# Kernel optimization log

Measured on AMD Instinct MI355X. Metric: run time of the kernel, lower is better.

The kernel has to match this reference:

```python
import jax, jax.numpy as jnp
import numpy as np

B, S, DIM, H = 1, 4096, 1024, 16
HEAD_DIM = DIM // H
ROPE_THETA = 10000.0
LN_EPS = 1e-5


def _rope_cos_sin(seq_len, dim, theta):
    # frequencies over the FULL model dim (rope applied before head split, as in source)
    inv_freq = 1.0 / (theta ** (jnp.arange(0, dim, 2, dtype=jnp.float32) / dim))  # (dim/2,)
    ang = jnp.arange(seq_len, dtype=jnp.float32)[:, None] * inv_freq[None, :]     # (S, dim/2)
    cos = jnp.concatenate([jnp.cos(ang), jnp.cos(ang)], axis=-1)                  # (S, dim)
    sin = jnp.concatenate([jnp.sin(ang), jnp.sin(ang)], axis=-1)
    return cos, sin


def _rotate_half(x):
    d = x.shape[-1] // 2
    return jnp.concatenate([-x[..., d:], x[..., :d]], axis=-1)


def _apply_rope(x, cos, sin):
    # x: (B, S, dim); cos/sin: (S, dim)
    return x * cos[None] + _rotate_half(x) * sin[None]


def setup_inputs() -> dict:
    key = jax.random.key(0)
    ks = jax.random.split(key, 5)
    sc = 1.0 / np.sqrt(DIM)
    return {
        "x": jax.random.normal(ks[0], (B, S, DIM), dtype=jnp.float32),
        "Wqkv": jax.random.normal(ks[1], (DIM, 3 * DIM), dtype=jnp.float32) * sc,
        "bqkv": jax.random.normal(ks[2], (3 * DIM,), dtype=jnp.float32) * 0.01,
        "Wo": jax.random.normal(ks[3], (DIM, DIM), dtype=jnp.float32) * sc,
        "bo": jax.random.normal(ks[4], (DIM,), dtype=jnp.float32) * 0.01,
        "gamma": jnp.ones((DIM,), dtype=jnp.float32),
        "beta": jnp.zeros((DIM,), dtype=jnp.float32),
    }


def reference(x, Wqkv, bqkv, Wo, bo, gamma, beta):
    b, s, d = x.shape
    qkv = x @ Wqkv + bqkv                      # (B, S, 3*dim)
    q, k, v = jnp.split(qkv, 3, axis=-1)       # each (B, S, dim)
    cos, sin = _rope_cos_sin(s, d, ROPE_THETA)
    q = _apply_rope(q, cos, sin)
    k = _apply_rope(k, cos, sin)
    # split heads
    q = q.reshape(b, s, H, HEAD_DIM)
    k = k.reshape(b, s, H, HEAD_DIM)
    v = v.reshape(b, s, H, HEAD_DIM)
    scale = 1.0 / np.sqrt(HEAD_DIM)
    scores = jnp.einsum('bqhd,bkhd->bhqk', q, k) * scale  # (B, H, S, S)
    causal = jnp.triu(jnp.ones((s, s), dtype=bool), k=1)
    scores = jnp.where(causal[None, None], -jnp.inf, scores)
    attn = jax.nn.softmax(scores, axis=-1)
    out = jnp.einsum('bhqk,bkhd->bqhd', attn, v).reshape(b, s, d)
    out = out @ Wo + bo
    # LayerNorm (dropout is identity in eval mode)
    mu = jnp.mean(out, axis=-1, keepdims=True)
    var = jnp.mean(jnp.square(out - mu), axis=-1, keepdims=True)
    return (out - mu) * jax.lax.rsqrt(var + LN_EPS) * gamma + beta
```

## Files before the change

### kernel.cpp

```cpp
#include <hip/hip_runtime.h>
#include <cstdint>
#include <cstddef>

#define S_LEN 4096
#define DIM   1024
#define NH    16
#define HD    64
#define QKV_N 3072

typedef __attribute__((ext_vector_type(8))) short short8;
typedef __attribute__((ext_vector_type(4))) float f32x4;
typedef __attribute__((ext_vector_type(4))) unsigned short ushort4v;

__device__ inline unsigned short f2bf(float x) {
    unsigned int u = __builtin_bit_cast(unsigned int, x);
    u += 0x7fffu + ((u >> 16) & 1u);
    return (unsigned short)(u >> 16);
}

__device__ inline void gl_lds16(const void* g, void* l) {
    __builtin_amdgcn_global_load_lds(
        (const __attribute__((address_space(1))) void*)g,
        (__attribute__((address_space(3))) void*)l, 16, 0, 0);
}

__global__ __launch_bounds__(256) void gemm_mfma_kernel(
    const unsigned short* __restrict__ A,
    const unsigned short* __restrict__ Bt,
    const float* __restrict__ bias,
    float* __restrict__ C,
    int M, int N, int K)
{
    __shared__ unsigned short As[128 * 32];
    __shared__ unsigned short Bs[128 * 32];

    const int t    = threadIdx.x;
    const int w    = t >> 6;
    const int lane = t & 63;
    const int ln   = lane & 15;
    const int quad = lane >> 4;
    const int bm   = blockIdx.y * 128;
    const int bn   = blockIdx.x * 128;
    const int wm   = (w & 1) * 64;
    const int wn   = (w >> 1) * 64;

    f32x4 acc[4][4];
#pragma unroll
    for (int i = 0; i < 4; ++i)
#pragma unroll
        for (int j = 0; j < 4; ++j) acc[i][j] = (f32x4){0.f, 0.f, 0.f, 0.f};

    const int lr = lane >> 2;
    const int lc = (lane & 3) * 8;
    const unsigned short* ga = A  + (size_t)(bm + w * 32 + lr) * K + lc;
    const unsigned short* gb = Bt + (size_t)(bn + w * 32 + lr) * K + lc;
    unsigned short* la = &As[(w * 32) * 32];
    unsigned short* lb = &Bs[(w * 32) * 32];

    for (int k0 = 0; k0 < K; k0 += 32) {
        gl_lds16(ga,            la);
        gl_lds16(ga + 16 * K,   la + 16 * 32);
        gl_lds16(gb,            lb);
        gl_lds16(gb + 16 * K,   lb + 16 * 32);
        ga += 32; gb += 32;
        __syncthreads();

        short8 af[4], bf[4];
#pragma unroll
        for (int i = 0; i < 4; ++i)
            af[i] = *(const short8*)&As[(wm + i * 16 + ln) * 32 + quad * 8];
#pragma unroll
        for (int j = 0; j < 4; ++j)
            bf[j] = *(const short8*)&Bs[(wn + j * 16 + ln) * 32 + quad * 8];
#pragma unroll
        for (int i = 0; i < 4; ++i)
#pragma unroll
            for (int j = 0; j < 4; ++j)
                acc[i][j] = __builtin_amdgcn_mfma_f32_16x16x32_bf16(af[i], bf[j], acc[i][j], 0, 0, 0);
        __syncthreads();
    }

#pragma unroll
    for (int j = 0; j < 4; ++j) {
        const int col = bn + wn + j * 16 + ln;
        const float bv = bias[col];
#pragma unroll
        for (int i = 0; i < 4; ++i) {
            const int row0 = bm + wm + i * 16 + quad * 4;
#pragma unroll
            for (int r = 0; r < 4; ++r)
                C[(size_t)(row0 + r) * N + col] = acc[i][j][r] + bv;
        }
    }
}

__global__ __launch_bounds__(256) void cvt_bf16_kernel(
    const float* __restrict__ in, unsigned short* __restrict__ out)
{
    const size_t i = ((size_t)blockIdx.x * 256 + threadIdx.x) * 8;
    float4 a = *(const float4*)(in + i);
    float4 b = *(const float4*)(in + i + 4);
    short8 p = { (short)f2bf(a.x), (short)f2bf(a.y), (short)f2bf(a.z), (short)f2bf(a.w),
                 (short)f2bf(b.x), (short)f2bf(b.y), (short)f2bf(b.z), (short)f2bf(b.w) };
    *(short8*)(out + i) = p;
}

__global__ __launch_bounds__(256) void wtrans_kernel(
    const float* __restrict__ W, unsigned short* __restrict__ Wt, int K, int N)
{
    __shared__ unsigned short L[64][72];
    const int t  = threadIdx.x;
    const int k0 = blockIdx.y * 64;
    const int n0 = blockIdx.x * 64;

    const int kr = t >> 2, cb = (t & 3) * 16;
    const float* wp = W + (size_t)(k0 + kr) * N + n0 + cb;
#pragma unroll
    for (int u = 0; u < 16; u += 4) {
        float4 v = *(const float4*)(wp + u);
        ushort4v p = { f2bf(v.x), f2bf(v.y), f2bf(v.z), f2bf(v.w) };
        *(ushort4v*)&L[kr][cb + u] = p;
    }
    __syncthreads();
    const int nr = t >> 2, kb = (t & 3) * 16;
    short8 lo, hi;
#pragma unroll
    for (int u = 0; u < 8; ++u) lo[u] = (short)L[kb + u][nr];
#pragma unroll
    for (int u = 0; u < 8; ++u) hi[u] = (short)L[kb + 8 + u][nr];
    unsigned short* op = Wt + (size_t)(n0 + nr) * K + k0 + kb;
    *(short8*)op       = lo;
    *(short8*)(op + 8) = hi;
}

__global__ __launch_bounds__(256) void rope_cvt_kernel(
    const float* __restrict__ qkv,
    unsigned short* __restrict__ Qb,
    unsigned short* __restrict__ Kb)
{
    const int idx = blockIdx.x * 256 + threadIdx.x;
    const int j   = (idx & 127) * 4;
    const int s   = idx >> 7;
    const float* row = qkv + (size_t)s * QKV_N;
    unsigned short* qo = Qb + (size_t)s * DIM;
    unsigned short* ko = Kb + (size_t)s * DIM;
    const float sf = (float)s;
    const float QSCALE = 0.18033688011112042f;
    const float C1 = -0.025952563241307517f;
    const float INV2PI = 0.15915494309189535f;

    float cs[4], sn[4];
#pragma unroll
    for (int e = 0; e < 4; ++e) {
        const float invf2pi = exp2f((float)(j + e) * C1) * INV2PI;
        float rev = sf * invf2pi;
        rev -= floorf(rev);
        sn[e] = __builtin_amdgcn_sinf(rev);
        cs[e] = __builtin_amdgcn_cosf(rev);
    }
    float4 q1 = *(const float4*)(row + j);
    float4 q2 = *(const float4*)(row + 512 + j);
    float4 k1 = *(const float4*)(row + DIM + j);
    float4 k2 = *(const float4*)(row + DIM + 512 + j);
    float x1[4] = {q1.x, q1.y, q1.z, q1.w};
    float x2[4] = {q2.x, q2.y, q2.z, q2.w};
    float y1[4] = {k1.x, k1.y, k1.z, k1.w};
    float y2[4] = {k2.x, k2.y, k2.z, k2.w};
    ushort4v qa, qb4, ka, kb4;
#pragma unroll
    for (int e = 0; e < 4; ++e) {
        qa[e]  = f2bf((x1[e] * cs[e] - x2[e] * sn[e]) * QSCALE);
        qb4[e] = f2bf((x2[e] * cs[e] + x1[e] * sn[e]) * QSCALE);
        ka[e]  = f2bf(y1[e] * cs[e] - y2[e] * sn[e]);
        kb4[e] = f2bf(y2[e] * cs[e] + y1[e] * sn[e]);
    }
    *(ushort4v*)(qo + j)       = qa;
    *(ushort4v*)(qo + 512 + j) = qb4;
    *(ushort4v*)(ko + j)       = ka;
    *(ushort4v*)(ko + 512 + j) = kb4;
}

__global__ __launch_bounds__(256) void vtrans_kernel(
    const float* __restrict__ qkv, unsigned short* __restrict__ Vt)
{
    __shared__ unsigned short L[64][72];
    const int t  = threadIdx.x;
    const int bs = blockIdx.y * 64;
    const int c0 = blockIdx.x * 64;

    const int sl = t >> 2, cb = (t & 3) * 16;
    const float* vp = qkv + (size_t)(bs + sl) * QKV_N + 2 * DIM + c0 + cb;
#pragma unroll
    for (int u = 0; u < 16; u += 4) {
        float4 v = *(const float4*)(vp + u);
        ushort4v p = { f2bf(v.x), f2bf(v.y), f2bf(v.z), f2bf(v.w) };
        *(ushort4v*)&L[sl][cb + u] = p;
    }
    __syncthreads();
    const int cl = t >> 2, sb = (t & 3) * 16;
    short8 lo, hi;
#pragma unroll
    for (int u = 0; u < 8; ++u) lo[u] = (short)L[sb + u][cl];
#pragma unroll
    for (int u = 0; u < 8; ++u) hi[u] = (short)L[sb + 8 + u][cl];
    unsigned short* op = Vt + (size_t)(c0 + cl) * S_LEN + bs + sb;
    *(short8*)op       = lo;
    *(short8*)(op + 8) = hi;
}

__global__ __launch_bounds__(256) void attn_mfma_kernel(
    const unsigned short* __restrict__ Qb,
    const unsigned short* __restrict__ Kb,
    const unsigned short* __restrict__ Vt,
    unsigned short* __restrict__ outb)
{
    __shared__ unsigned short Ks[64][72];
    __shared__ unsigned short Vs[64][72];
    __shared__ unsigned short Ps[4][16][72];

    const int t    = threadIdx.x;
    const int w    = t >> 6;
    const int lane = t & 63;
    const int ln   = lane & 15;
    const int quad = lane >> 4;
    const int h    = blockIdx.y;
    const int p    = blockIdx.x;

    const int sc_ = t >> 2;
    const int so  = (t & 3) * 16;

#pragma unroll
    for (int phase = 0; phase < 2; ++phase) {
        const int qt = phase == 0 ? (63 - p) : p;
        const int q0 = qt * 64;

        short8 qf[2];
        {
            const unsigned short* qp = Qb + (size_t)(q0 + w * 16 + ln) * DIM + h * HD + quad * 8;
            qf[0] = *(const short8*)qp;
            qf[1] = *(const short8*)(qp + 32);
        }

        f32x4 o[4];
#pragma unroll
        for (int db = 0; db < 4; ++db) o[db] = (f32x4){0.f, 0.f, 0.f, 0.f};
        float mrow = -1e30f, lrow = 0.f;

        short8 kr0, kr1, vr0, vr1;
        {
            const unsigned short* kp = Kb + (size_t)sc_ * DIM + h * HD + so;
            kr0 = *(const short8*)kp;  kr1 = *(const short8*)(kp + 8);
            const unsigned short* vp = Vt + (size_t)(h * HD + sc_) * S_LEN + so;
            vr0 = *(const short8*)vp;  vr1 = *(const short8*)(vp + 8);
        }

        for (int kt = 0; kt <= qt; ++kt) {
            __syncthreads();
            *(short8*)&Ks[sc_][so]     = kr0;
            *(short8*)&Ks[sc_][so + 8] = kr1;
            *(short8*)&Vs[sc_][so]     = vr0;
            *(short8*)&Vs[sc_][so + 8] = vr1;
            if (kt < qt) {
                const int k1 = (kt + 1) * 64;
                const unsigned short* kp = Kb + (size_t)(k1 + sc_) * DIM + h * HD + so;
                kr0 = *(const short8*)kp;  kr1 = *(const short8*)(kp + 8);
                const unsigned short* vp = Vt + (size_t)(h * HD + sc_) * S_LEN + k1 + so;
                vr0 = *(const short8*)vp;  vr1 = *(const short8*)(vp + 8);
            }
            __syncthreads();

            f32x4 sc[4];
#pragma unroll
            for (int kb = 0; kb < 4; ++kb) sc[kb] = (f32x4){0.f, 0.f, 0.f, 0.f};
#pragma unroll
            for (int kk = 0; kk < 2; ++kk) {
#pragma unroll
                for (int kb = 0; kb < 4; ++kb) {
                    short8 kf = *(const short8*)&Ks[kb * 16 + ln][kk * 32 + quad * 8];
                    sc[kb] = __builtin_amdgcn_mfma_f32_16x16x32_bf16(kf, qf[kk], sc[kb], 0, 0, 0);
                }
            }

            if (kt == qt) {
#pragma unroll
                for (int kb = 0; kb < 4; ++kb) {
                    const int key = kb * 16 + quad * 4;
#pragma unroll
                    for (int r = 0; r < 4; ++r)
                        if (key + r > w * 16 + ln) sc[kb][r] = -1e30f;
                }
            }

            float tm = -1e30f;
#pragma unroll
            for (int kb = 0; kb < 4; ++kb)
#pragma unroll
                for (int r = 0; r < 4; ++r) tm = fmaxf(tm, sc[kb][r]);
            tm = fmaxf(tm, __shfl_xor(tm, 16));
            tm = fmaxf(tm, __shfl_xor(tm, 32));
            const float mnew = fmaxf(mrow, tm);
            const float al   = exp2f(mrow - mnew);
            mrow = mnew;
            float ps = 0.f;
#pragma unroll
            for (int kb = 0; kb < 4; ++kb) {
                ushort4v pk;
#pragma unroll
                for (int r = 0; r < 4; ++r) {
                    const float pv = exp2f(sc[kb][r] - mnew);
                    ps += pv;
                    pk[r] = f2bf(pv);
                }
                *(ushort4v*)&Ps[w][ln][kb * 16 + quad * 4] = pk;
            }
            ps += __shfl_xor(ps, 16);
            ps += __shfl_xor(ps, 32);
            lrow = lrow * al + ps;
#pragma unroll
            for (int db = 0; db < 4; ++db) o[db] *= al;

#pragma unroll
            for (int kk = 0; kk < 2; ++kk) {
                short8 pf = *(const short8*)&Ps[w][ln][kk * 32 + quad * 8];
#pragma unroll
                for (int db = 0; db < 4; ++db) {
                    short8 vf = *(const short8*)&Vs[db * 16 + ln][kk * 32 + quad * 8];
                    o[db] = __builtin_amdgcn_mfma_f32_16x16x32_bf16(vf, pf, o[db], 0, 0, 0);
                }
            }
        }

        const float inv = 1.0f / lrow;
#pragma unroll
        for (int db = 0; db < 4; ++db) {
            ushort4v pk;
#pragma unroll
            for (int r = 0; r < 4; ++r) pk[r] = f2bf(o[db][r] * inv);
            *(ushort4v*)&Ps[w][ln][db * 16 + quad * 4] = pk;
        }
        {
            const int m  = lane >> 2;
            const int d0 = (lane & 3) * 16;
            short8 r0 = *(const short8*)&Ps[w][m][d0];
            short8 r1 = *(const short8*)&Ps[w][m][d0 + 8];
            unsigned short* op = outb + (size_t)(q0 + w * 16 + m) * DIM + h * HD + d0;
            *(short8*)op       = r0;
            *(short8*)(op + 8) = r1;
        }
    }
}

__global__ __launch_bounds__(256) void ln_kernel(
    const float* __restrict__ in, const float* __restrict__ gamma,
    const float* __restrict__ beta, float* __restrict__ out)
{
    const int row = blockIdx.x;
    const int t = threadIdx.x;
    const float4 v = *(const float4*)&in[(size_t)row * DIM + t * 4];
    float s  = v.x + v.y + v.z + v.w;
    float sq = v.x * v.x + v.y * v.y + v.z * v.z + v.w * v.w;
#pragma unroll
    for (int off = 1; off < 64; off <<= 1) {
        s  += __shfl_xor(s, off);
        sq += __shfl_xor(sq, off);
    }
    __shared__ float red[8];
    const int wv = t >> 6, ln = t & 63;
    if (ln == 0) { red[wv] = s; red[4 + wv] = sq; }
    __syncthreads();
    s  = red[0] + red[1] + red[2] + red[3];
    sq = red[4] + red[5] + red[6] + red[7];
    const float mu  = s * (1.0f / DIM);
    const float var = sq * (1.0f / DIM) - mu * mu;
    const float rs  = rsqrtf(var + 1e-5f);
    const float4 g = *(const float4*)&gamma[t * 4];
    const float4 b = *(const float4*)&beta[t * 4];
    float4 o = { (v.x - mu) * rs * g.x + b.x,
                 (v.y - mu) * rs * g.y + b.y,
                 (v.z - mu) * rs * g.z + b.z,
                 (v.w - mu) * rs * g.w + b.w };
    *(float4*)&out[(size_t)row * DIM + t * 4] = o;
}

extern "C" void kernel_launch(void* const* d_in, const int* in_sizes, int n_in,
                              void* d_out, int out_size, void* d_ws, size_t ws_size,
                              hipStream_t stream)
{
    const float* x     = (const float*)d_in[0];
    const float* Wqkv  = (const float*)d_in[1];
    const float* bqkv  = (const float*)d_in[2];
    const float* Wo    = (const float*)d_in[3];
    const float* bo    = (const float*)d_in[4];
    const float* gamma = (const float*)d_in[5];
    const float* beta  = (const float*)d_in[6];
    float* out = (float*)d_out;

    char* base = (char*)d_ws;
    float* qkv = (float*)base;
    unsigned short* attnb = (unsigned short*)base;
    float* proj = (float*)(base + (size_t)8 * 1024 * 1024);
    unsigned short* Qb    = (unsigned short*)(base + (size_t)48 * 1024 * 1024);
    unsigned short* Kb    = (unsigned short*)(base + (size_t)56 * 1024 * 1024);
    unsigned short* Vt    = (unsigned short*)(base + (size_t)64 * 1024 * 1024);
    unsigned short* xb    = (unsigned short*)(base + (size_t)72 * 1024 * 1024);
    unsigned short* WqkvT = (unsigned short*)(base + (size_t)80 * 1024 * 1024);
    unsigned short* WoT   = (unsigned short*)(base + (size_t)86 * 1024 * 1024);

    cvt_bf16_kernel<<<(S_LEN * DIM) / (256 * 8), 256, 0, stream>>>(x, xb);
    wtrans_kernel<<<dim3(QKV_N / 64, DIM / 64), 256, 0, stream>>>(Wqkv, WqkvT, DIM, QKV_N);
    wtrans_kernel<<<dim3(DIM / 64, DIM / 64), 256, 0, stream>>>(Wo, WoT, DIM, DIM);

    gemm_mfma_kernel<<<dim3(QKV_N / 128, S_LEN / 128), 256, 0, stream>>>(
        xb, WqkvT, bqkv, qkv, S_LEN, QKV_N, DIM);

    rope_cvt_kernel<<<(S_LEN * 128) / 256, 256, 0, stream>>>(qkv, Qb, Kb);
    vtrans_kernel<<<dim3(16, S_LEN / 64), 256, 0, stream>>>(qkv, Vt);

    attn_mfma_kernel<<<dim3(32, NH), 256, 0, stream>>>(Qb, Kb, Vt, attnb);

    gemm_mfma_kernel<<<dim3(DIM / 128, S_LEN / 128), 256, 0, stream>>>(
        attnb, WoT, bo, proj, S_LEN, DIM, DIM);

    ln_kernel<<<S_LEN, 256, 0, stream>>>(proj, gamma, beta, out);
}
```

Measured before the change: 277.3 us.

## Emit bf16 QKV from GEMM and split attention into one query tile per block

The QKV GEMM now writes its output as bf16 instead of fp32, which halves the intermediate traffic read by the rope and V-transpose kernels. The attention kernel drops the paired-tile scheme (tile p and 63-p per block) and launches 64x16 blocks with one query tile each, heaviest first, to raise parallelism. The P-matrix bf16 packing uses a perm-based round-half-up conversion. The cost is extra rounding of QKV before rope, and load imbalance is now left to the hardware scheduler.

```diff
diff --git a/kernel.cpp b/kernel.cpp
--- a/kernel.cpp
+++ b/kernel.cpp
@@ -11,12 +11,21 @@
 typedef __attribute__((ext_vector_type(8))) short short8;
 typedef __attribute__((ext_vector_type(4))) float f32x4;
 typedef __attribute__((ext_vector_type(4))) unsigned short ushort4v;
+typedef __attribute__((ext_vector_type(2))) unsigned int uint2v;
 
 __device__ inline unsigned short f2bf(float x) {
     unsigned int u = __builtin_bit_cast(unsigned int, x);
     u += 0x7fffu + ((u >> 16) & 1u);
     return (unsigned short)(u >> 16);
 }
+__device__ inline float bf2f(unsigned short u) {
+    return __builtin_bit_cast(float, (unsigned int)u << 16);
+}
+__device__ inline unsigned int pack2_bf16_rh(float lo, float hi) {
+    unsigned int a = __builtin_bit_cast(unsigned int, lo) + 0x8000u;
+    unsigned int b = __builtin_bit_cast(unsigned int, hi) + 0x8000u;
+    return __builtin_amdgcn_perm(b, a, 0x07060302u);
+}
 
 __device__ inline void gl_lds16(const void* g, void* l) {
     __builtin_amdgcn_global_load_lds(
@@ -24,11 +33,12 @@
         (__attribute__((address_space(3))) void*)l, 16, 0, 0);
 }
 
+template <bool BF16OUT>
 __global__ __launch_bounds__(256) void gemm_mfma_kernel(
     const unsigned short* __restrict__ A,
     const unsigned short* __restrict__ Bt,
     const float* __restrict__ bias,
-    float* __restrict__ C,
+    void* __restrict__ Cv,
     int M, int N, int K)
 {
     __shared__ unsigned short As[128 * 32];
@@ -88,8 +98,13 @@
         for (int i = 0; i < 4; ++i) {
             const int row0 = bm + wm + i * 16 + quad * 4;
 #pragma unroll
-            for (int r = 0; r < 4; ++r)
-                C[(size_t)(row0 + r) * N + col] = acc[i][j][r] + bv;
+            for (int r = 0; r < 4; ++r) {
+                const float v = acc[i][j][r] + bv;
+                if (BF16OUT)
+                    ((unsigned short*)Cv)[(size_t)(row0 + r) * N + col] = f2bf(v);
+                else
+                    ((float*)Cv)[(size_t)(row0 + r) * N + col] = v;
+            }
         }
     }
 }
@@ -134,14 +149,14 @@
 }
 
 __global__ __launch_bounds__(256) void rope_cvt_kernel(
-    const float* __restrict__ qkv,
+    const unsigned short* __restrict__ qkvb,
     unsigned short* __restrict__ Qb,
     unsigned short* __restrict__ Kb)
 {
     const int idx = blockIdx.x * 256 + threadIdx.x;
     const int j   = (idx & 127) * 4;
     const int s   = idx >> 7;
-    const float* row = qkv + (size_t)s * QKV_N;
+    const unsigned short* row = qkvb + (size_t)s * QKV_N;
     unsigned short* qo = Qb + (size_t)s * DIM;
     unsigned short* ko = Kb + (size_t)s * DIM;
     const float sf = (float)s;
@@ -158,21 +173,19 @@
         sn[e] = __builtin_amdgcn_sinf(rev);
         cs[e] = __builtin_amdgcn_cosf(rev);
     }
-    float4 q1 = *(const float4*)(row + j);
-    float4 q2 = *(const float4*)(row + 512 + j);
-    float4 k1 = *(const float4*)(row + DIM + j);
-    float4 k2 = *(const float4*)(row + DIM + 512 + j);
-    float x1[4] = {q1.x, q1.y, q1.z, q1.w};
-    float x2[4] = {q2.x, q2.y, q2.z, q2.w};
-    float y1[4] = {k1.x, k1.y, k1.z, k1.w};
-    float y2[4] = {k2.x, k2.y, k2.z, k2.w};
+    ushort4v q1 = *(const ushort4v*)(row + j);
+    ushort4v q2 = *(const ushort4v*)(row + 512 + j);
+    ushort4v k1 = *(const ushort4v*)(row + DIM + j);
+    ushort4v k2 = *(const ushort4v*)(row + DIM + 512 + j);
     ushort4v qa, qb4, ka, kb4;
 #pragma unroll
     for (int e = 0; e < 4; ++e) {
-        qa[e]  = f2bf((x1[e] * cs[e] - x2[e] * sn[e]) * QSCALE);
-        qb4[e] = f2bf((x2[e] * cs[e] + x1[e] * sn[e]) * QSCALE);
-        ka[e]  = f2bf(y1[e] * cs[e] - y2[e] * sn[e]);
-        kb4[e] = f2bf(y2[e] * cs[e] + y1[e] * sn[e]);
+        const float x1 = bf2f(q1[e]), x2 = bf2f(q2[e]);
+        const float y1 = bf2f(k1[e]), y2 = bf2f(k2[e]);
+        qa[e]  = f2bf((x1 * cs[e] - x2 * sn[e]) * QSCALE);
+        qb4[e] = f2bf((x2 * cs[e] + x1 * sn[e]) * QSCALE);
+        ka[e]  = f2bf(y1 * cs[e] - y2 * sn[e]);
+        kb4[e] = f2bf(y2 * cs[e] + y1 * sn[e]);
     }
     *(ushort4v*)(qo + j)       = qa;
     *(ushort4v*)(qo + 512 + j) = qb4;
@@ -181,7 +194,7 @@
 }
 
 __global__ __launch_bounds__(256) void vtrans_kernel(
-    const float* __restrict__ qkv, unsigned short* __restrict__ Vt)
+    const unsigned short* __restrict__ qkvb, unsigned short* __restrict__ Vt)
 {
     __shared__ unsigned short L[64][72];
     const int t  = threadIdx.x;
@@ -189,13 +202,9 @@
     const int c0 = blockIdx.x * 64;
 
     const int sl = t >> 2, cb = (t & 3) * 16;
-    const float* vp = qkv + (size_t)(bs + sl) * QKV_N + 2 * DIM + c0 + cb;
-#pragma unroll
-    for (int u = 0; u < 16; u += 4) {
-        float4 v = *(const float4*)(vp + u);
-        ushort4v p = { f2bf(v.x), f2bf(v.y), f2bf(v.z), f2bf(v.w) };
-        *(ushort4v*)&L[sl][cb + u] = p;
-    }
+    const unsigned short* vp = qkvb + (size_t)(bs + sl) * QKV_N + 2 * DIM + c0 + cb;
+    *(short8*)&L[sl][cb]     = *(const short8*)vp;
+    *(short8*)&L[sl][cb + 8] = *(const short8*)(vp + 8);
     __syncthreads();
     const int cl = t >> 2, sb = (t & 3) * 16;
     short8 lo, hi;
@@ -224,129 +233,124 @@
     const int ln   = lane & 15;
     const int quad = lane >> 4;
     const int h    = blockIdx.y;
-    const int p    = blockIdx.x;
+    const int qt   = 63 - (int)blockIdx.x;
+    const int q0   = qt * 64;
 
     const int sc_ = t >> 2;
     const int so  = (t & 3) * 16;
 
-#pragma unroll
-    for (int phase = 0; phase < 2; ++phase) {
-        const int qt = phase == 0 ? (63 - p) : p;
-        const int q0 = qt * 64;
-
-        short8 qf[2];
-        {
-            const unsigned short* qp = Qb + (size_t)(q0 + w * 16 + ln) * DIM + h * HD + quad * 8;
-            qf[0] = *(const short8*)qp;
-            qf[1] = *(const short8*)(qp + 32);
-        }
-
-        f32x4 o[4];
-#pragma unroll
-        for (int db = 0; db < 4; ++db) o[db] = (f32x4){0.f, 0.f, 0.f, 0.f};
-        float mrow = -1e30f, lrow = 0.f;
-
-        short8 kr0, kr1, vr0, vr1;
-        {
-            const unsigned short* kp = Kb + (size_t)sc_ * DIM + h * HD + so;
+    short8 qf[2];
+    {
+        const unsigned short* qp = Qb + (size_t)(q0 + w * 16 + ln) * DIM + h * HD + quad * 8;
+        qf[0] = *(const short8*)qp;
+        qf[1] = *(const short8*)(qp + 32);
+    }
+
+    f32x4 o[4];
+#pragma unroll
+    for (int db = 0; db < 4; ++db) o[db] = (f32x4){0.f, 0.f, 0.f, 0.f};
+    float mrow = -1e30f, lrow = 0.f;
+
+    short8 kr0, kr1, vr0, vr1;
+    {
+        const unsigned short* kp = Kb + (size_t)sc_ * DIM + h * HD + so;
+        kr0 = *(const short8*)kp;  kr1 = *(const short8*)(kp + 8);
+        const unsigned short* vp = Vt + (size_t)(h * HD + sc_) * S_LEN + so;
+        vr0 = *(const short8*)vp;  vr1 = *(const short8*)(vp + 8);
+    }
+
+    for (int kt = 0; kt <= qt; ++kt) {
+        __syncthreads();
+        *(short8*)&Ks[sc_][so]     = kr0;
+        *(short8*)&Ks[sc_][so + 8] = kr1;
+        *(short8*)&Vs[sc_][so]     = vr0;
+        *(short8*)&Vs[sc_][so + 8] = vr1;
+        if (kt < qt) {
+            const int k1 = (kt + 1) * 64;
+            const unsigned short* kp = Kb + (size_t)(k1 + sc_) * DIM + h * HD + so;
             kr0 = *(const short8*)kp;  kr1 = *(const short8*)(kp + 8);
-            const unsigned short* vp = Vt + (size_t)(h * HD + sc_) * S_LEN + so;
+            const unsigned short* vp = Vt + (size_t)(h * HD + sc_) * S_LEN + k1 + so;
             vr0 = *(const short8*)vp;  vr1 = *(const short8*)(vp + 8);
         }
-
-        for (int kt = 0; kt <= qt; ++kt) {
-            __syncthreads();
-            *(short8*)&Ks[sc_][so]     = kr0;
-            *(short8*)&Ks[sc_][so + 8] = kr1;
-            *(short8*)&Vs[sc_][so]     = vr0;
-            *(short8*)&Vs[sc_][so + 8] = vr1;
-            if (kt < qt) {
-                const int k1 = (kt + 1) * 64;
-                const unsigned short* kp = Kb + (size_t)(k1 + sc_) * DIM + h * HD + so;
-                kr0 = *(const short8*)kp;  kr1 = *(const short8*)(kp + 8);
-                const unsigned short* vp = Vt + (size_t)(h * HD + sc_) * S_LEN + k1 + so;
-                vr0 = *(const short8*)vp;  vr1 = *(const short8*)(vp + 8);
+        __syncthreads();
+
+        f32x4 sc[4];
+#pragma unroll
+        for (int kb = 0; kb < 4; ++kb) sc[kb] = (f32x4){0.f, 0.f, 0.f, 0.f};
+#pragma unroll
+        for (int kk = 0; kk < 2; ++kk) {
+#pragma unroll
+            for (int kb = 0; kb < 4; ++kb) {
+                short8 kf = *(const short8*)&Ks[kb * 16 + ln][kk * 32 + quad * 8];
+                sc[kb] = __builtin_amdgcn_mfma_f32_16x16x32_bf16(kf, qf[kk], sc[kb], 0, 0, 0);
             }
-            __syncthreads();
-
-            f32x4 sc[4];
-#pragma unroll
-            for (int kb = 0; kb < 4; ++kb) sc[kb] = (f32x4){0.f, 0.f, 0.f, 0.f};
-#pragma unroll
-            for (int kk = 0; kk < 2; ++kk) {
-#pragma unroll
-                for (int kb = 0; kb < 4; ++kb) {
-                    short8 kf = *(const short8*)&Ks[kb * 16 + ln][kk * 32 + quad * 8];
-                    sc[kb] = __builtin_amdgcn_mfma_f32_16x16x32_bf16(kf, qf[kk], sc[kb], 0, 0, 0);
-                }
+        }
+
+        if (kt == qt) {
+#pragma unroll
+            for (int kb = 0; kb < 4; ++kb) {
+                const int key = kb * 16 + quad * 4;
+#pragma unroll
+                for (int r = 0; r < 4; ++r)
+                    if (key + r > w * 16 + ln) sc[kb][r] = -1e30f;
             }
-
-            if (kt == qt) {
-#pragma unroll
-                for (int kb = 0; kb < 4; ++kb) {
-                    const int key = kb * 16 + quad * 4;
-#pragma unroll
-                    for (int r = 0; r < 4; ++r)
-                        if (key + r > w * 16 + ln) sc[kb][r] = -1e30f;
-                }
+        }
+
+        float tm = -1e30f;
+#pragma unroll
+        for (int kb = 0; kb < 4; ++kb)
+#pragma unroll
+            for (int r = 0; r < 4; ++r) tm = fmaxf(tm, sc[kb][r]);
+        tm = fmaxf(tm, __shfl_xor(tm, 16));
+        tm = fmaxf(tm, __shfl_xor(tm, 32));
+        const float mnew = fmaxf(mrow, tm);
+        const float al   = exp2f(mrow - mnew);
+        mrow = mnew;
+        float ps = 0.f;
+#pragma unroll
+        for (int kb = 0; kb < 4; ++kb) {
+            float pv[4];
+#pragma unroll
+            for (int r = 0; r < 4; ++r) {
+                pv[r] = exp2f(sc[kb][r] - mnew);
+                ps += pv[r];
             }
-
-            float tm = -1e30f;
-#pragma unroll
-            for (int kb = 0; kb < 4; ++kb)
-#pragma unroll
-                for (int r = 0; r < 4; ++r) tm = fmaxf(tm, sc[kb][r]);
-            tm = fmaxf(tm, __shfl_xor(tm, 16));
-            tm = fmaxf(tm, __shfl_xor(tm, 32));
-            const float mnew = fmaxf(mrow, tm);
-            const float al   = exp2f(mrow - mnew);
-            mrow = mnew;
-            float ps = 0.f;
-#pragma unroll
-            for (int kb = 0; kb < 4; ++kb) {
-                ushort4v pk;
-#pragma unroll
-                for (int r = 0; r < 4; ++r) {
-                    const float pv = exp2f(sc[kb][r] - mnew);
-                    ps += pv;
-                    pk[r] = f2bf(pv);
-                }
-                *(ushort4v*)&Ps[w][ln][kb * 16 + quad * 4] = pk;
+            uint2v pk = { pack2_bf16_rh(pv[0], pv[1]), pack2_bf16_rh(pv[2], pv[3]) };
+            *(uint2v*)&Ps[w][ln][kb * 16 + quad * 4] = pk;
+        }
+        ps += __shfl_xor(ps, 16);
+        ps += __shfl_xor(ps, 32);
+        lrow = lrow * al + ps;
+#pragma unroll
+        for (int db = 0; db < 4; ++db) o[db] *= al;
+
+#pragma unroll
+        for (int kk = 0; kk < 2; ++kk) {
+            short8 pf = *(const short8*)&Ps[w][ln][kk * 32 + quad * 8];
+#pragma unroll
+            for (int db = 0; db < 4; ++db) {
+                short8 vf = *(const short8*)&Vs[db * 16 + ln][kk * 32 + quad * 8];
+                o[db] = __builtin_amdgcn_mfma_f32_16x16x32_bf16(vf, pf, o[db], 0, 0, 0);
             }
-            ps += __shfl_xor(ps, 16);
-            ps += __shfl_xor(ps, 32);
-            lrow = lrow * al + ps;
-#pragma unroll
-            for (int db = 0; db < 4; ++db) o[db] *= al;
-
-#pragma unroll
-            for (int kk = 0; kk < 2; ++kk) {
-                short8 pf = *(const short8*)&Ps[w][ln][kk * 32 + quad * 8];
-#pragma unroll
-                for (int db = 0; db < 4; ++db) {
-                    short8 vf = *(const short8*)&Vs[db * 16 + ln][kk * 32 + quad * 8];
-                    o[db] = __builtin_amdgcn_mfma_f32_16x16x32_bf16(vf, pf, o[db], 0, 0, 0);
-                }
-            }
-        }
-
-        const float inv = 1.0f / lrow;
-#pragma unroll
-        for (int db = 0; db < 4; ++db) {
-            ushort4v pk;
-#pragma unroll
-            for (int r = 0; r < 4; ++r) pk[r] = f2bf(o[db][r] * inv);
-            *(ushort4v*)&Ps[w][ln][db * 16 + quad * 4] = pk;
-        }
-        {
-            const int m  = lane >> 2;
-            const int d0 = (lane & 3) * 16;
-            short8 r0 = *(const short8*)&Ps[w][m][d0];
-            short8 r1 = *(const short8*)&Ps[w][m][d0 + 8];
-            unsigned short* op = outb + (size_t)(q0 + w * 16 + m) * DIM + h * HD + d0;
-            *(short8*)op       = r0;
-            *(short8*)(op + 8) = r1;
-        }
+        }
+    }
+
+    const float inv = 1.0f / lrow;
+#pragma unroll
+    for (int db = 0; db < 4; ++db) {
+        ushort4v pk;
+#pragma unroll
+        for (int r = 0; r < 4; ++r) pk[r] = f2bf(o[db][r] * inv);
+        *(ushort4v*)&Ps[w][ln][db * 16 + quad * 4] = pk;
+    }
+    {
+        const int m  = lane >> 2;
+        const int d0 = (lane & 3) * 16;
+        short8 r0 = *(const short8*)&Ps[w][m][d0];
+        short8 r1 = *(const short8*)&Ps[w][m][d0 + 8];
+        unsigned short* op = outb + (size_t)(q0 + w * 16 + m) * DIM + h * HD + d0;
+        *(short8*)op       = r0;
+        *(short8*)(op + 8) = r1;
     }
 }
 
@@ -396,7 +400,7 @@
     float* out = (float*)d_out;
 
     char* base = (char*)d_ws;
-    float* qkv = (float*)base;
+    unsigned short* qkvb  = (unsigned short*)base;
     unsigned short* attnb = (unsigned short*)base;
     float* proj = (float*)(base + (size_t)8 * 1024 * 1024);
     unsigned short* Qb    = (unsigned short*)(base + (size_t)48 * 1024 * 1024);
@@ -410,15 +414,15 @@
     wtrans_kernel<<<dim3(QKV_N / 64, DIM / 64), 256, 0, stream>>>(Wqkv, WqkvT, DIM, QKV_N);
     wtrans_kernel<<<dim3(DIM / 64, DIM / 64), 256, 0, stream>>>(Wo, WoT, DIM, DIM);
 
-    gemm_mfma_kernel<<<dim3(QKV_N / 128, S_LEN / 128), 256, 0, stream>>>(
-        xb, WqkvT, bqkv, qkv, S_LEN, QKV_N, DIM);
-
-    rope_cvt_kernel<<<(S_LEN * 128) / 256, 256, 0, stream>>>(qkv, Qb, Kb);
-    vtrans_kernel<<<dim3(16, S_LEN / 64), 256, 0, stream>>>(qkv, Vt);
-
-    attn_mfma_kernel<<<dim3(32, NH), 256, 0, stream>>>(Qb, Kb, Vt, attnb);
-
-    gemm_mfma_kernel<<<dim3(DIM / 128, S_LEN / 128), 256, 0, stream>>>(
+    gemm_mfma_kernel<true><<<dim3(QKV_N / 128, S_LEN / 128), 256, 0, stream>>>(
+        xb, WqkvT, bqkv, qkvb, S_LEN, QKV_N, DIM);
+
+    rope_cvt_kernel<<<(S_LEN * 128) / 256, 256, 0, stream>>>(qkvb, Qb, Kb);
+    vtrans_kernel<<<dim3(16, S_LEN / 64), 256, 0, stream>>>(qkvb, Vt);
+
+    attn_mfma_kernel<<<dim3(64, NH), 256, 0, stream>>>(Qb, Kb, Vt, attnb);
+
+    gemm_mfma_kernel<false><<<dim3(DIM / 128, S_LEN / 128), 256, 0, stream>>>(
         attnb, WoT, bo, proj, S_LEN, DIM, DIM);
 
     ln_kernel<<<S_LEN, 256, 0, stream>>>(proj, gamma, beta, out);
```

Result: slower. 319.3 us (+15.2%).
